# Performance work log

Measured on AMD Instinct MI355X. Metric: run time of the kernel, lower is better.

The kernel has to match this reference:

```python
import jax, jax.numpy as jnp
import numpy as np

B, S, D_MODEL, H = 2, 2048, 512, 8
D_HEAD = D_MODEL // H  # 64; d_qk == d_model here


def setup_inputs() -> dict:
    key = jax.random.key(0)
    ks = jax.random.split(key, 7)
    sc = 1.0 / np.sqrt(D_MODEL)
    return {
        "x": jax.random.normal(ks[0], (B, S, D_MODEL), dtype=jnp.float32),
        "Wqk_w": jax.random.normal(ks[1], (2 * D_MODEL, D_MODEL), dtype=jnp.float32) * sc,
        "Wqk_b": jax.random.normal(ks[2], (2 * D_MODEL,), dtype=jnp.float32) * 0.01,
        "Wv_w": jax.random.normal(ks[3], (D_MODEL, D_MODEL), dtype=jnp.float32) * sc,
        "Wv_b": jax.random.normal(ks[4], (D_MODEL,), dtype=jnp.float32) * 0.01,
        "Wo_w": jax.random.normal(ks[5], (D_MODEL, D_MODEL), dtype=jnp.float32) * sc,
        "Wo_b": jax.random.normal(ks[6], (D_MODEL,), dtype=jnp.float32) * 0.01,
    }


def reference(x, Wqk_w, Wqk_b, Wv_w, Wv_b, Wo_w, Wo_b):
    b, s, _ = x.shape
    # projections
    qk = x @ Wqk_w.T + Wqk_b              # [B,S,2*d_qk]
    v = x @ Wv_w.T + Wv_b                 # [B,S,d_model]
    qk = qk.reshape(b, s, 2, H, D_HEAD)   # (two h d) layout
    v = v.reshape(b, s, H, D_HEAD)
    q, k = qk[:, :, 0], qk[:, :, 1]
    # generalized linear attention feature map: elu(x)+1
    q = jax.nn.elu(q) + 1.0
    k = jax.nn.elu(k) + 1.0
    scores = jnp.einsum('bthd,bshd->bhts', q, k)          # [B,H,T,S]
    mask = jnp.tril(jnp.ones((s, s), dtype=scores.dtype))  # causal multiplicative mask
    scores = scores * mask
    nu = scores.sum(axis=-1, keepdims=True)               # row normalizer
    attention = scores / nu
    context = jnp.einsum('bhts,bshd->bthd', attention, v)  # [B,T,H,D]
    out = context.reshape(b, s, D_MODEL) @ Wo_w.T + Wo_b
    return out
```

## Files before the change

### kernel.cpp

```cpp
#include <hip/hip_runtime.h>
#include <math.h>

#define B_N 2
#define S_N 2048
#define DM  512
#define H_N 8
#define DH  64
#define NC  32
#define CH  64

typedef __bf16 bf16x8 __attribute__((ext_vector_type(8)));
typedef float  f32x4  __attribute__((ext_vector_type(4)));

__device__ __forceinline__ unsigned short f2bf(float f) {
    unsigned int u = __float_as_uint(f);
    u += 0x7FFFu + ((u >> 16) & 1u);
    return (unsigned short)(u >> 16);
}

__device__ __forceinline__ void gload16(const void* g, void* l) {
    __builtin_amdgcn_global_load_lds(
        (const __attribute__((address_space(1))) unsigned int*)g,
        (__attribute__((address_space(3))) unsigned int*)l, 16, 0, 0);
}

__global__ __launch_bounds__(256) void convert_bf16(
    const float* __restrict__ x,  const float* __restrict__ wqk,
    const float* __restrict__ wv, const float* __restrict__ wo,
    unsigned short* __restrict__ xb,  unsigned short* __restrict__ wqkb,
    unsigned short* __restrict__ wvb, unsigned short* __restrict__ wob)
{
    int gid = blockIdx.x * 256 + threadIdx.x;
    const float* src; unsigned short* dst; int off;
    if (gid < 524288)      { src = x;   dst = xb;   off = gid; }
    else if (gid < 655360) { src = wqk; dst = wqkb; off = gid - 524288; }
    else if (gid < 720896) { src = wv;  dst = wvb;  off = gid - 655360; }
    else                   { src = wo;  dst = wob;  off = gid - 720896; }
    float4 v = ((const float4*)src)[off];
    ushort4 r; r.x = f2bf(v.x); r.y = f2bf(v.y); r.z = f2bf(v.z); r.w = f2bf(v.w);
    ((ushort4*)dst)[off] = r;
}

__global__ __launch_bounds__(256) void gemm_qkv_fused(
    const unsigned short* __restrict__ xb,
    const unsigned short* __restrict__ Wqkb,
    const unsigned short* __restrict__ Wvb,
    const float* __restrict__ bqk, const float* __restrict__ bv,
    unsigned short* __restrict__ qb, unsigned short* __restrict__ kb_,
    unsigned short* __restrict__ vtb,
    float* __restrict__ Asum, float* __restrict__ zsum)
{
    __shared__ unsigned short Alds[2 * 64 * 32];
    __shared__ unsigned short Blds[2 * 128 * 32];
    __shared__ unsigned short ktT[64 * 72];
    __shared__ unsigned short vtT[64 * 72];

    const int tid = threadIdx.x;
    const int w = tid >> 6, l = tid & 63;
    const int wm = w >> 1, wn = w & 1;
    const int lane15 = l & 15, quad = l >> 4;
    const int bx = blockIdx.x;
    const int m0 = blockIdx.y * 64;
    const int isq = (bx < 4);
    const int h = isq ? 0 : (bx - 4);

    const int srow = w * 16 + (l >> 2);
    const int skof = (l & 3) << 3;

    f32x4 acc[2][4];
    #pragma unroll
    for (int i = 0; i < 2; i++)
        #pragma unroll
        for (int j = 0; j < 4; j++) acc[i][j] = (f32x4){0.f, 0.f, 0.f, 0.f};

    for (int k0 = 0; k0 < DM; k0 += 64) {
        __syncthreads();
        gload16(&xb[(size_t)(m0 + srow) * DM + k0 + skof],      (char*)Alds + w * 1024);
        gload16(&xb[(size_t)(m0 + srow) * DM + k0 + 32 + skof], (char*)Alds + 4096 + w * 1024);
        if (isq) {
            gload16(&Wqkb[(size_t)(bx * 128 + srow) * DM + k0 + skof],           (char*)Blds + w * 1024);
            gload16(&Wqkb[(size_t)(bx * 128 + 64 + srow) * DM + k0 + skof],      (char*)Blds + 4096 + w * 1024);
            gload16(&Wqkb[(size_t)(bx * 128 + srow) * DM + k0 + 32 + skof],      (char*)Blds + 8192 + w * 1024);
            gload16(&Wqkb[(size_t)(bx * 128 + 64 + srow) * DM + k0 + 32 + skof], (char*)Blds + 12288 + w * 1024);
        } else {
            gload16(&Wqkb[(size_t)(512 + h * 64 + srow) * DM + k0 + skof],       (char*)Blds + w * 1024);
            gload16(&Wvb[(size_t)(h * 64 + srow) * DM + k0 + skof],              (char*)Blds + 4096 + w * 1024);
            gload16(&Wqkb[(size_t)(512 + h * 64 + srow) * DM + k0 + 32 + skof],  (char*)Blds + 8192 + w * 1024);
            gload16(&Wvb[(size_t)(h * 64 + srow) * DM + k0 + 32 + skof],         (char*)Blds + 12288 + w * 1024);
        }
        __syncthreads();

        #pragma unroll
        for (int s = 0; s < 2; s++) {
            bf16x8 af[2], bfr[4];
            #pragma unroll
            for (int i = 0; i < 2; i++)
                af[i] = *(bf16x8*)&Alds[s * 2048 + (wm * 32 + i * 16 + lane15) * 32 + quad * 8];
            #pragma unroll
            for (int j = 0; j < 4; j++)
                bfr[j] = *(bf16x8*)&Blds[s * 4096 + (wn * 64 + j * 16 + lane15) * 32 + quad * 8];
            #pragma unroll
            for (int i = 0; i < 2; i++)
                #pragma unroll
                for (int j = 0; j < 4; j++)
                    acc[i][j] = __builtin_amdgcn_mfma_f32_16x16x32_bf16(af[i], bfr[j], acc[i][j], 0, 0, 0);
        }
    }

    const int bbu = m0 >> 11;
    const int t0  = m0 & (S_N - 1);
    const int c0  = t0 >> 6;

    if (isq) {
        #pragma unroll
        for (int i = 0; i < 2; i++) {
            #pragma unroll
            for (int rg = 0; rg < 4; rg++) {
                int m = m0 + wm * 32 + i * 16 + quad * 4 + rg;
                int bb = m >> 11, t = m & (S_N - 1);
                #pragma unroll
                for (int j = 0; j < 4; j++) {
                    int n = bx * 128 + wn * 64 + j * 16 + lane15;
                    float val = acc[i][j][rg] + bqk[n];
                    val = (val > 0.f) ? (val + 1.f) : __expf(val);
                    qb[(((size_t)bb * H_N + (n >> 6)) * S_N + t) * DH + (n & 63)] = f2bf(val);
                }
            }
        }
        return;
    }

    #pragma unroll
    for (int i = 0; i < 2; i++) {
        #pragma unroll
        for (int rg = 0; rg < 4; rg++) {
            int tl = wm * 32 + i * 16 + quad * 4 + rg;
            int t  = t0 + tl;
            #pragma unroll
            for (int j = 0; j < 4; j++) {
                int col = j * 16 + lane15;
                if (wn == 0) {
                    float val = acc[i][j][rg] + bqk[512 + h * 64 + col];
                    val = (val > 0.f) ? (val + 1.f) : __expf(val);
                    unsigned short us = f2bf(val);
                    kb_[(((size_t)bbu * H_N + h) * S_N + t) * DH + col] = us;
                    ktT[col * 72 + tl] = us;
                } else {
                    float val = acc[i][j][rg] + bv[h * 64 + col];
                    vtT[col * 72 + tl] = f2bf(val);
                }
            }
        }
    }
    __syncthreads();

    {
        size_t vbase = (((size_t)bbu * H_N + h) * DH) * S_N + t0;
        #pragma unroll
        for (int it = 0; it < 2; it++) {
            int idx = it * 2048 + tid * 8;
            int d = idx >> 6, tt = idx & 63;
            *(bf16x8*)&vtb[vbase + (size_t)d * S_N + tt] = *(bf16x8*)&vtT[d * 72 + tt];
        }
    }

    {
        int blk = ((bbu * H_N + h) * NC) + c0;
        bf16x8 va[2];
        #pragma unroll
        for (int s = 0; s < 2; s++)
            va[s] = *(bf16x8*)&vtT[(w * 16 + lane15) * 72 + s * 32 + quad * 8];
        f32x4 sacc[4];
        #pragma unroll
        for (int j = 0; j < 4; j++) sacc[j] = (f32x4){0.f, 0.f, 0.f, 0.f};
        #pragma unroll
        for (int j = 0; j < 4; j++)
            #pragma unroll
            for (int s = 0; s < 2; s++) {
                bf16x8 kB = *(bf16x8*)&ktT[(j * 16 + lane15) * 72 + s * 32 + quad * 8];
                sacc[j] = __builtin_amdgcn_mfma_f32_16x16x32_bf16(va[s], kB, sacc[j], 0, 0, 0);
            }
        #pragma unroll
        for (int j = 0; j < 4; j++)
            #pragma unroll
            for (int rg = 0; rg < 4; rg++)
                Asum[(size_t)blk * 4096 + (w * 16 + quad * 4 + rg) * 64 + j * 16 + lane15] = sacc[j][rg];
    }

    if (tid < 64) {
        float z = 0.f;
        #pragma unroll
        for (int p = 0; p < 8; p++) {
            bf16x8 kk = *(bf16x8*)&ktT[tid * 72 + p * 8];
            #pragma unroll
            for (int e = 0; e < 8; e++) z += (float)kk[e];
        }
        zsum[(size_t)((bbu * H_N + h) * NC + c0) * 64 + tid] = z;
    }
}

__global__ __launch_bounds__(256) void scan_states(
    const float* __restrict__ Asum, float* __restrict__ zsum,
    unsigned short* __restrict__ Sptb)
{
    const int gid = blockIdx.x * 256 + threadIdx.x;
    const int bh = gid / 4160;
    const int r  = gid % 4160;
    if (r < 4096) {
        size_t base = (size_t)bh * NC * 4096 + r;
        float vals[NC];
        #pragma unroll
        for (int c = 0; c < NC; c++) vals[c] = Asum[base + (size_t)c * 4096];
        float acc = 0.f;
        #pragma unroll
        for (int c = 0; c < NC; c++) {
            float tmp = vals[c];
            Sptb[base + (size_t)c * 4096] = f2bf(acc);
            acc += tmp;
        }
    } else {
        int d = r - 4096;
        size_t base = (size_t)bh * NC * 64 + d;
        float vals[NC];
        #pragma unroll
        for (int c = 0; c < NC; c++) vals[c] = zsum[base + (size_t)c * 64];
        float acc = 0.f;
        #pragma unroll
        for (int c = 0; c < NC; c++) {
            float tmp = vals[c];
            zsum[base + (size_t)c * 64] = acc;
            acc += tmp;
        }
    }
}

__global__ __launch_bounds__(256) void attn_mfma(
    const unsigned short* __restrict__ qb, const unsigned short* __restrict__ kb_,
    const unsigned short* __restrict__ vtb, const unsigned short* __restrict__ Sptb,
    const float* __restrict__ zsum, unsigned short* __restrict__ ctxb)
{
    __shared__ __align__(16) unsigned short P[64 * 72];
    __shared__ float nupart[64][4];

    const int blk = blockIdx.x;
    const int bh = blk >> 5, c = blk & 31;
    const int b = bh >> 3, h = bh & 7;
    const int tid = threadIdx.x;
    const int w = tid >> 6, l = tid & 63;
    const int lane15 = l & 15, quad = l >> 4;

    const unsigned short* qc  = qb  + (size_t)bh * S_N * DH + c * CH * DH;
    const unsigned short* kc  = kb_ + (size_t)bh * S_N * DH + c * CH * DH;
    const unsigned short* vtc = vtb + (size_t)bh * DH * S_N + c * CH;
    const unsigned short* spc = Sptb + (size_t)blk * 4096;
    const float* zc = zsum + (size_t)blk * 64;

    bf16x8 af[2];
    #pragma unroll
    for (int s = 0; s < 2; s++)
        af[s] = *(const bf16x8*)&qc[(w * 16 + lane15) * DH + s * 32 + quad * 8];

    f32x4 sacc[4];
    #pragma unroll
    for (int j = 0; j < 4; j++) sacc[j] = (f32x4){0.f, 0.f, 0.f, 0.f};
    #pragma unroll
    for (int j = 0; j < 4; j++)
        #pragma unroll
        for (int s = 0; s < 2; s++) {
            bf16x8 bk = *(const bf16x8*)&kc[(j * 16 + lane15) * DH + s * 32 + quad * 8];
            sacc[j] = __builtin_amdgcn_mfma_f32_16x16x32_bf16(af[s], bk, sacc[j], 0, 0, 0);
        }

    const int r0 = w * 16 + quad * 4;
    #pragma unroll
    for (int j = 0; j < 4; j++) {
        int u = j * 16 + lane15;
        #pragma unroll
        for (int rg = 0; rg < 4; rg++) {
            int rr = r0 + rg;
            float v = (u <= rr) ? sacc[j][rg] : 0.f;
            P[rr * 72 + u] = f2bf(v);
        }
    }
    __syncthreads();

    const int tl = tid >> 2, part = tid & 3;
    float nup = 0.f;
    {
        bf16x8 p0 = *(const bf16x8*)&P[tl * 72 + part * 16];
        bf16x8 p1 = *(const bf16x8*)&P[tl * 72 + part * 16 + 8];
        bf16x8 q0 = *(const bf16x8*)&qc[tl * DH + part * 16];
        bf16x8 q1 = *(const bf16x8*)&qc[tl * DH + part * 16 + 8];
        #pragma unroll
        for (int i = 0; i < 8; i++) {
            nup += (float)p0[i] + (float)p1[i];
            nup += (float)q0[i] * zc[part * 16 + i];
            nup += (float)q1[i] * zc[part * 16 + 8 + i];
        }
    }
    nupart[tl][part] = nup;
    __syncthreads();

    bf16x8 pa[2];
    #pragma unroll
    for (int s = 0; s < 2; s++)
        pa[s] = *(const bf16x8*)&P[(w * 16 + lane15) * 72 + s * 32 + quad * 8];

    f32x4 acc[4];
    #pragma unroll
    for (int j = 0; j < 4; j++) acc[j] = (f32x4){0.f, 0.f, 0.f, 0.f};
    #pragma unroll
    for (int j = 0; j < 4; j++)
        #pragma unroll
        for (int s = 0; s < 2; s++) {
            bf16x8 bv8 = *(const bf16x8*)&vtc[(size_t)(j * 16 + lane15) * S_N + s * 32 + quad * 8];
            acc[j] = __builtin_amdgcn_mfma_f32_16x16x32_bf16(pa[s], bv8, acc[j], 0, 0, 0);
            bf16x8 bs = *(const bf16x8*)&spc[(j * 16 + lane15) * 64 + s * 32 + quad * 8];
            acc[j] = __builtin_amdgcn_mfma_f32_16x16x32_bf16(af[s], bs, acc[j], 0, 0, 0);
        }

    #pragma unroll
    for (int rg = 0; rg < 4; rg++) {
        int rr = r0 + rg;
        float nu = nupart[rr][0] + nupart[rr][1] + nupart[rr][2] + nupart[rr][3];
        float inv = 1.f / nu;
        size_t obase = ((size_t)b * S_N + c * CH + rr) * DM + h * DH;
        #pragma unroll
        for (int j = 0; j < 4; j++)
            ctxb[obase + j * 16 + lane15] = f2bf(acc[j][rg] * inv);
    }
}

__global__ __launch_bounds__(256) void gemm_out_mfma(
    const unsigned short* __restrict__ ctxb,
    const unsigned short* __restrict__ Wob,
    const float* __restrict__ bo, float* __restrict__ out)
{
    __shared__ unsigned short Alds[2 * 64 * 32];
    __shared__ unsigned short Blds[2 * 64 * 32];
    const int tid = threadIdx.x;
    const int w = tid >> 6, l = tid & 63;
    const int wm = w >> 1, wn = w & 1;
    const int lane15 = l & 15, quad = l >> 4;
    const int n0 = blockIdx.x * 64;
    const int m0 = blockIdx.y * 64;

    const int srow = w * 16 + (l >> 2);
    const int skof = (l & 3) << 3;

    f32x4 acc[2][2];
    #pragma unroll
    for (int i = 0; i < 2; i++)
        #pragma unroll
        for (int j = 0; j < 2; j++) acc[i][j] = (f32x4){0.f, 0.f, 0.f, 0.f};

    for (int k0 = 0; k0 < DM; k0 += 64) {
        __syncthreads();
        gload16(&ctxb[(size_t)(m0 + srow) * DM + k0 + skof],      (char*)Alds + w * 1024);
        gload16(&ctxb[(size_t)(m0 + srow) * DM + k0 + 32 + skof], (char*)Alds + 4096 + w * 1024);
        gload16(&Wob[(size_t)(n0 + srow) * DM + k0 + skof],       (char*)Blds + w * 1024);
        gload16(&Wob[(size_t)(n0 + srow) * DM + k0 + 32 + skof],  (char*)Blds + 4096 + w * 1024);
        __syncthreads();

        #pragma unroll
        for (int s = 0; s < 2; s++) {
            bf16x8 af2[2], bfr[2];
            #pragma unroll
            for (int i = 0; i < 2; i++)
                af2[i] = *(bf16x8*)&Alds[s * 2048 + (wm * 32 + i * 16 + lane15) * 32 + quad * 8];
            #pragma unroll
            for (int j = 0; j < 2; j++)
                bfr[j] = *(bf16x8*)&Blds[s * 2048 + (wn * 32 + j * 16 + lane15) * 32 + quad * 8];
            #pragma unroll
            for (int i = 0; i < 2; i++)
                #pragma unroll
                for (int j = 0; j < 2; j++)
                    acc[i][j] = __builtin_amdgcn_mfma_f32_16x16x32_bf16(af2[i], bfr[j], acc[i][j], 0, 0, 0);
        }
    }

    #pragma unroll
    for (int i = 0; i < 2; i++) {
        #pragma unroll
        for (int rg = 0; rg < 4; rg++) {
            int m = m0 + wm * 32 + i * 16 + quad * 4 + rg;
            #pragma unroll
            for (int j = 0; j < 2; j++) {
                int n = n0 + wn * 32 + j * 16 + lane15;
                out[(size_t)m * DM + n] = acc[i][j][rg] + bo[n];
            }
        }
    }
}

extern "C" void kernel_launch(void* const* d_in, const int* in_sizes, int n_in,
                              void* d_out, int out_size, void* d_ws, size_t ws_size,
                              hipStream_t stream)
{
    const float* x   = (const float*)d_in[0];
    const float* Wqk = (const float*)d_in[1];
    const float* bqk = (const float*)d_in[2];
    const float* Wv  = (const float*)d_in[3];
    const float* bv  = (const float*)d_in[4];
    const float* Wo  = (const float*)d_in[5];
    const float* bo  = (const float*)d_in[6];
    float* out = (float*)d_out;

    const size_t NTOK = (size_t)B_N * S_N * DM;
    float* Asum = (float*)d_ws;
    float* zsum = Asum + NTOK;
    unsigned short* xb   = (unsigned short*)(zsum + 32768);
    unsigned short* Wqkb = xb   + NTOK;
    unsigned short* Wvb  = Wqkb + 524288;
    unsigned short* Wob  = Wvb  + 262144;
    unsigned short* qb   = Wob  + 262144;
    unsigned short* kb_  = qb   + NTOK;
    unsigned short* vtb  = kb_  + NTOK;
    unsigned short* Sptb = vtb  + NTOK;
    unsigned short* ctxb = Sptb + NTOK;

    convert_bf16  <<<dim3(3072),   256, 0, stream>>>(x, Wqk, Wv, Wo, xb, Wqkb, Wvb, Wob);
    gemm_qkv_fused<<<dim3(12, 64), 256, 0, stream>>>(xb, Wqkb, Wvb, bqk, bv, qb, kb_, vtb, Asum, zsum);
    scan_states   <<<dim3(260),    256, 0, stream>>>(Asum, zsum, Sptb);
    attn_mfma     <<<dim3(512),    256, 0, stream>>>(qb, kb_, vtb, Sptb, zsum, ctxb);
    gemm_out_mfma <<<dim3(8, 64),  256, 0, stream>>>(ctxb, Wob, bo, out);
}
```

Measured before the change: 113.6 us.

## Fuse prefix-state scan into attention kernel with XCD-aware block mapping

Removes the separate scan_states launch. Each attention block now sums the per-chunk state matrices and normalizer vectors of all earlier chunks itself and stages the result as bf16 in shared memory. It also remaps block IDs so that blocks sharing a head land on the same XCD, which should improve L2 reuse of Asum. The cost is redundant work: block c reads and sums c chunk states (up to 31×16KB), giving quadratic total traffic in place of a linear scan, plus one fewer launch and one fewer bf16 round trip through global memory.

```diff
diff --git a/kernel.cpp b/kernel.cpp
--- a/kernel.cpp
+++ b/kernel.cpp
@@ -199,51 +199,20 @@
     }
 }
 
-__global__ __launch_bounds__(256) void scan_states(
-    const float* __restrict__ Asum, float* __restrict__ zsum,
-    unsigned short* __restrict__ Sptb)
-{
-    const int gid = blockIdx.x * 256 + threadIdx.x;
-    const int bh = gid / 4160;
-    const int r  = gid % 4160;
-    if (r < 4096) {
-        size_t base = (size_t)bh * NC * 4096 + r;
-        float vals[NC];
-        #pragma unroll
-        for (int c = 0; c < NC; c++) vals[c] = Asum[base + (size_t)c * 4096];
-        float acc = 0.f;
-        #pragma unroll
-        for (int c = 0; c < NC; c++) {
-            float tmp = vals[c];
-            Sptb[base + (size_t)c * 4096] = f2bf(acc);
-            acc += tmp;
-        }
-    } else {
-        int d = r - 4096;
-        size_t base = (size_t)bh * NC * 64 + d;
-        float vals[NC];
-        #pragma unroll
-        for (int c = 0; c < NC; c++) vals[c] = zsum[base + (size_t)c * 64];
-        float acc = 0.f;
-        #pragma unroll
-        for (int c = 0; c < NC; c++) {
-            float tmp = vals[c];
-            zsum[base + (size_t)c * 64] = acc;
-            acc += tmp;
-        }
-    }
-}
-
 __global__ __launch_bounds__(256) void attn_mfma(
     const unsigned short* __restrict__ qb, const unsigned short* __restrict__ kb_,
-    const unsigned short* __restrict__ vtb, const unsigned short* __restrict__ Sptb,
+    const unsigned short* __restrict__ vtb, const float* __restrict__ Asum,
     const float* __restrict__ zsum, unsigned short* __restrict__ ctxb)
 {
     __shared__ __align__(16) unsigned short P[64 * 72];
+    __shared__ __align__(16) unsigned short Spre[64 * 72];
     __shared__ float nupart[64][4];
-
-    const int blk = blockIdx.x;
-    const int bh = blk >> 5, c = blk & 31;
+    __shared__ float zc_s[64];
+
+    const int bid = blockIdx.x;
+    const int xcd = bid & 7, idx = bid >> 3;
+    const int bh = xcd + 8 * (idx & 1);
+    const int c  = idx >> 1;
     const int b = bh >> 3, h = bh & 7;
     const int tid = threadIdx.x;
     const int w = tid >> 6, l = tid & 63;
@@ -252,8 +221,36 @@
     const unsigned short* qc  = qb  + (size_t)bh * S_N * DH + c * CH * DH;
     const unsigned short* kc  = kb_ + (size_t)bh * S_N * DH + c * CH * DH;
     const unsigned short* vtc = vtb + (size_t)bh * DH * S_N + c * CH;
-    const unsigned short* spc = Sptb + (size_t)blk * 4096;
-    const float* zc = zsum + (size_t)blk * 64;
+
+    {
+        const float* abase = Asum + (size_t)bh * NC * 4096;
+        const int e = tid * 16;
+        float4 a0 = {0,0,0,0}, a1 = {0,0,0,0}, a2 = {0,0,0,0}, a3 = {0,0,0,0};
+        for (int cc = 0; cc < c; cc++) {
+            const float4* p = (const float4*)(abase + (size_t)cc * 4096 + e);
+            float4 p0 = p[0], p1 = p[1], p2 = p[2], p3 = p[3];
+            a0.x += p0.x; a0.y += p0.y; a0.z += p0.z; a0.w += p0.w;
+            a1.x += p1.x; a1.y += p1.y; a1.z += p1.z; a1.w += p1.w;
+            a2.x += p2.x; a2.y += p2.y; a2.z += p2.z; a2.w += p2.w;
+            a3.x += p3.x; a3.y += p3.y; a3.z += p3.z; a3.w += p3.w;
+        }
+        const int d2 = e >> 6, d1 = e & 63;
+        ushort4 u0 = {f2bf(a0.x), f2bf(a0.y), f2bf(a0.z), f2bf(a0.w)};
+        ushort4 u1 = {f2bf(a1.x), f2bf(a1.y), f2bf(a1.z), f2bf(a1.w)};
+        ushort4 u2 = {f2bf(a2.x), f2bf(a2.y), f2bf(a2.z), f2bf(a2.w)};
+        ushort4 u3 = {f2bf(a3.x), f2bf(a3.y), f2bf(a3.z), f2bf(a3.w)};
+        *(ushort4*)&Spre[d2 * 72 + d1]      = u0;
+        *(ushort4*)&Spre[d2 * 72 + d1 + 4]  = u1;
+        *(ushort4*)&Spre[d2 * 72 + d1 + 8]  = u2;
+        *(ushort4*)&Spre[d2 * 72 + d1 + 12] = u3;
+
+        if (tid < 64) {
+            const float* zbase = zsum + (size_t)bh * NC * 64 + tid;
+            float z = 0.f;
+            for (int cc = 0; cc < c; cc++) z += zbase[cc * 64];
+            zc_s[tid] = z;
+        }
+    }
 
     bf16x8 af[2];
     #pragma unroll
@@ -294,8 +291,8 @@
         #pragma unroll
         for (int i = 0; i < 8; i++) {
             nup += (float)p0[i] + (float)p1[i];
-            nup += (float)q0[i] * zc[part * 16 + i];
-            nup += (float)q1[i] * zc[part * 16 + 8 + i];
+            nup += (float)q0[i] * zc_s[part * 16 + i];
+            nup += (float)q1[i] * zc_s[part * 16 + 8 + i];
         }
     }
     nupart[tl][part] = nup;
@@ -315,7 +312,7 @@
         for (int s = 0; s < 2; s++) {
             bf16x8 bv8 = *(const bf16x8*)&vtc[(size_t)(j * 16 + lane15) * S_N + s * 32 + quad * 8];
             acc[j] = __builtin_amdgcn_mfma_f32_16x16x32_bf16(pa[s], bv8, acc[j], 0, 0, 0);
-            bf16x8 bs = *(const bf16x8*)&spc[(j * 16 + lane15) * 64 + s * 32 + quad * 8];
+            bf16x8 bs = *(const bf16x8*)&Spre[(j * 16 + lane15) * 72 + s * 32 + quad * 8];
             acc[j] = __builtin_amdgcn_mfma_f32_16x16x32_bf16(af[s], bs, acc[j], 0, 0, 0);
         }
 
@@ -416,12 +413,10 @@
     unsigned short* qb   = Wob  + 262144;
     unsigned short* kb_  = qb   + NTOK;
     unsigned short* vtb  = kb_  + NTOK;
-    unsigned short* Sptb = vtb  + NTOK;
-    unsigned short* ctxb = Sptb + NTOK;
+    unsigned short* ctxb = vtb  + NTOK;
 
     convert_bf16  <<<dim3(3072),   256, 0, stream>>>(x, Wqk, Wv, Wo, xb, Wqkb, Wvb, Wob);
     gemm_qkv_fused<<<dim3(12, 64), 256, 0, stream>>>(xb, Wqkb, Wvb, bqk, bv, qb, kb_, vtb, Asum, zsum);
-    scan_states   <<<dim3(260),    256, 0, stream>>>(Asum, zsum, Sptb);
-    attn_mfma     <<<dim3(512),    256, 0, stream>>>(qb, kb_, vtb, Sptb, zsum, ctxb);
+    attn_mfma     <<<dim3(512),    256, 0, stream>>>(qb, kb_, vtb, Asum, zsum, ctxb);
     gemm_out_mfma <<<dim3(8, 64),  256, 0, stream>>>(ctxb, Wob, bo, out);
 }
```

Measured after the change: 121.2 us. 6.7% more time.
